# Optimization experiments

Measured on AMD Instinct MI355X. Metric: run time of the kernel, lower is better.

The kernel has to match this reference:

```python
import jax, jax.numpy as jnp
import numpy as np

B, S, D, E, K = 4, 2048, 1024, 8, 2
DF = 4 * D


def setup_inputs() -> dict:
    key = jax.random.key(0)
    ks = jax.random.split(key, 7)
    x = jax.random.normal(ks[0], (B, S, D), dtype=jnp.float32)
    Wr = jax.random.normal(ks[1], (D, E), dtype=jnp.float32) * 0.02
    br = jnp.zeros((E,), dtype=jnp.float32)
    W1 = jax.random.normal(ks[2], (E, D, DF), dtype=jnp.float32) * 0.02
    b1 = jnp.zeros((E, DF), dtype=jnp.float32)
    W2 = jax.random.normal(ks[3], (E, DF, D), dtype=jnp.float32) * 0.02
    b2 = jnp.zeros((E, D), dtype=jnp.float32)
    return {"x": x, "Wr": Wr, "br": br, "W1": W1, "b1": b1, "W2": W2, "b2": b2}


def reference(x, Wr, br, W1, b1, W2, b2):
    # Router: softmax gates then top-k
    gates = jax.nn.softmax(x @ Wr + br, axis=-1)               # [B,S,E]
    topk_vals, topk_idx = jax.lax.top_k(gates, K)              # [B,S,K]

    # Per-(token, expert) combine weight: gate value if expert selected else 0
    onehot = jax.nn.one_hot(topk_idx, E, dtype=gates.dtype)    # [B,S,K,E]
    combine = jnp.sum(onehot * topk_vals[..., None], axis=2)   # [B,S,E]

    # Expert MLPs (loop over fixed small expert count, fully vectorized per expert)
    output = jnp.zeros_like(x)
    for e in range(E):
        h = jax.nn.gelu(x @ W1[e] + b1[e], approximate=False)  # [B,S,4D]
        y = h @ W2[e] + b2[e]                                  # [B,S,D]
        output = output + combine[..., e:e + 1] * y

    # Load-balancing aux loss (dispatch mask: 1.0 where expert selected)
    dispatch = jnp.max(onehot, axis=2)                         # [B,S,E]
    mean_gates = gates.mean(axis=(0, 1))
    mean_dispatch = dispatch.mean(axis=(0, 1))
    aux_loss = jnp.sum(mean_gates * mean_dispatch) * E / (B * S)
    return output, aux_loss
```

## Files before the change

### kernel.cpp

```cpp
#include <hip/hip_runtime.h>
#include <hip/hip_bf16.h>
#include <hip/hip_fp16.h>

typedef _Float16 f16;
typedef _Float16 half8 __attribute__((ext_vector_type(8)));
typedef _Float16 half4 __attribute__((ext_vector_type(4)));
typedef float   floatx4 __attribute__((ext_vector_type(4)));

#define N_TOK   8192
#define D_DIM   1024
#define E_NUM   8
#define DF_DIM  4096
#define MAX_SLOTS 17408
#define MAX_RT    136

#define MI_COUNT  0
#define MI_CURSOR 8
#define MI_OFF    16
#define MI_TOTAL  25
#define MI_RTE    26
#define MI_SUMG   168

__device__ __forceinline__ void gld_lds16(const void* g, void* l) {
    __builtin_amdgcn_global_load_lds(
        (__attribute__((address_space(1))) const void*)g,
        (__attribute__((address_space(3))) void*)l, 16, 0, 0);
}

__device__ __forceinline__ float gelu_f(float v) {
    float u = 0.7978845608028654f * v * (1.0f + 0.044715f * v * v);
    float t = __expf(-2.0f * fabsf(u));
    float th = (1.0f - t) / (1.0f + t);
    th = (u >= 0.f) ? th : -th;
    return 0.5f * v * (1.0f + th);
}


__device__ __forceinline__ void transpose_tile(
    const float* __restrict__ src, f16* __restrict__ dst, int R, int C,
    int rb, int cb, float* tile )
{
    const int tid = threadIdx.x;
#pragma unroll
    for (int j = 0; j < 4; ++j) {
        int lin = j * 1024 + tid * 4;
        int r = lin >> 6, c = lin & 63;
        float4 v = *(const float4*)(src + (size_t)(rb + r) * C + (cb + c));
        tile[r * 65 + c + 0] = v.x; tile[r * 65 + c + 1] = v.y;
        tile[r * 65 + c + 2] = v.z; tile[r * 65 + c + 3] = v.w;
    }
    __syncthreads();
#pragma unroll
    for (int j = 0; j < 4; ++j) {
        int lin = j * 1024 + tid * 4;
        int c = lin >> 6, r = lin & 63;
        half4 o = { (f16)tile[(r + 0) * 65 + c], (f16)tile[(r + 1) * 65 + c],
                    (f16)tile[(r + 2) * 65 + c], (f16)tile[(r + 3) * 65 + c] };
        *(half4*)(dst + (size_t)(cb + c) * R + (rb + r)) = o;
    }
}

__global__ __launch_bounds__(256) void prep_kernel(
    const float* __restrict__ W1, const float* __restrict__ W2,
    f16* __restrict__ W1t, f16* __restrict__ W2t,
    const float* __restrict__ x, const float* __restrict__ Wr,
    const float* __restrict__ br,
    int* __restrict__ topk_idx, float* __restrict__ topk_w,
    int* __restrict__ meta, f16* __restrict__ xh)
{
    __shared__ float tile[64 * 65];
    __shared__ float blk_sg[E_NUM];
    __shared__ int   blk_cnt[E_NUM];

    const int bid = blockIdx.x;
    if (bid < 8192) {
        const int cx = bid & 63, ry = (bid >> 6) & 15, ez = bid >> 10;
        transpose_tile(W1 + (size_t)ez * D_DIM * DF_DIM,
                       W1t + (size_t)ez * D_DIM * DF_DIM,
                       D_DIM, DF_DIM, ry * 64, cx * 64, tile);
        return;
    }
    if (bid < 16384) {
        const int id = bid - 8192;
        const int cx = id & 15, ry = (id >> 4) & 63, ez = id >> 10;
        transpose_tile(W2 + (size_t)ez * D_DIM * DF_DIM,
                       W2t + (size_t)ez * D_DIM * DF_DIM,
                       DF_DIM, D_DIM, ry * 64, cx * 64, tile);
        return;
    }

    const int rb = bid - 16384;
    const int w = threadIdx.x >> 6, l = threadIdx.x & 63;
    if (threadIdx.x < E_NUM) { blk_sg[threadIdx.x] = 0.f; blk_cnt[threadIdx.x] = 0; }
    __syncthreads();

    for (int it = 0; it < 4; ++it) {
        const int t = rb * 16 + w * 4 + it;
        const float* xr = x + (size_t)t * D_DIM + l * 16;
        float acc[E_NUM] = {0.f,0.f,0.f,0.f,0.f,0.f,0.f,0.f};
        f16 hx[16];
#pragma unroll
        for (int i = 0; i < 16; i += 4) {
            float4 xv = *(const float4*)(xr + i);
            const float xs[4] = {xv.x, xv.y, xv.z, xv.w};
#pragma unroll
            for (int jj = 0; jj < 4; ++jj) {
                hx[i + jj] = (f16)xs[jj];
                int d = l * 16 + i + jj;
                float4 w0 = *(const float4*)(Wr + (size_t)d * 8);
                float4 w1 = *(const float4*)(Wr + (size_t)d * 8 + 4);
                acc[0] += xs[jj] * w0.x; acc[1] += xs[jj] * w0.y;
                acc[2] += xs[jj] * w0.z; acc[3] += xs[jj] * w0.w;
                acc[4] += xs[jj] * w1.x; acc[5] += xs[jj] * w1.y;
                acc[6] += xs[jj] * w1.z; acc[7] += xs[jj] * w1.w;
            }
        }
        f16* xo = xh + (size_t)t * D_DIM + l * 16;
        *(half8*)(xo)     = *(const half8*)&hx[0];
        *(half8*)(xo + 8) = *(const half8*)&hx[8];
#pragma unroll
        for (int e = 0; e < E_NUM; ++e) {
#pragma unroll
            for (int off = 32; off > 0; off >>= 1)
                acc[e] += __shfl_down(acc[e], off);
        }
        if (l == 0) {
            float lg[E_NUM], g[E_NUM];
            float mx = -1e30f;
#pragma unroll
            for (int e = 0; e < E_NUM; ++e) { lg[e] = acc[e] + br[e]; mx = fmaxf(mx, lg[e]); }
            float sum = 0.f;
#pragma unroll
            for (int e = 0; e < E_NUM; ++e) { g[e] = __expf(lg[e] - mx); sum += g[e]; }
            float inv = 1.f / sum;
#pragma unroll
            for (int e = 0; e < E_NUM; ++e) g[e] *= inv;
            int e1 = 0; float v1 = g[0];
#pragma unroll
            for (int e = 1; e < E_NUM; ++e) if (g[e] > v1) { v1 = g[e]; e1 = e; }
            int e2 = -1; float v2 = -1.f;
#pragma unroll
            for (int e = 0; e < E_NUM; ++e) if (e != e1 && g[e] > v2) { v2 = g[e]; e2 = e; }
            topk_idx[t * 2 + 0] = e1; topk_idx[t * 2 + 1] = e2;
            topk_w[t * 2 + 0] = v1;   topk_w[t * 2 + 1] = v2;
#pragma unroll
            for (int e = 0; e < E_NUM; ++e) atomicAdd(&blk_sg[e], g[e]);
            atomicAdd(&blk_cnt[e1], 1); atomicAdd(&blk_cnt[e2], 1);
        }
    }
    __syncthreads();
    if (threadIdx.x < E_NUM) {
        atomicAdd((float*)(meta + MI_SUMG) + threadIdx.x, blk_sg[threadIdx.x]);
        atomicAdd(meta + MI_COUNT + threadIdx.x, blk_cnt[threadIdx.x]);
    }
}

__global__ __launch_bounds__(256) void scan_kernel(int* __restrict__ meta, float* __restrict__ out_aux)
{
    __shared__ int offs[E_NUM + 1];
    const int tid = threadIdx.x;
    if (tid == 0) {
        int off = 0;
        for (int e = 0; e < E_NUM; ++e) {
            meta[MI_OFF + e] = off;
            offs[e] = off;
            int cnt = meta[MI_COUNT + e];
            off += ((cnt + 127) >> 7) << 7;
        }
        meta[MI_OFF + E_NUM] = off;
        offs[E_NUM] = off;
        meta[MI_TOTAL] = off >> 7;
        const float* sg = (const float*)(meta + MI_SUMG);
        float aux = 0.f;
        for (int e = 0; e < E_NUM; ++e)
            aux += (sg[e] / (float)N_TOK) * ((float)meta[MI_COUNT + e] / (float)N_TOK);
        out_aux[0] = aux * (float)E_NUM / (float)N_TOK;
    }
    __syncthreads();
    const int total = offs[E_NUM] >> 7;
    for (int rt = tid; rt < total; rt += 256) {
        int row = rt << 7, e = 0;
#pragma unroll
        for (int k = 1; k < E_NUM; ++k) if (row >= offs[k]) e = k;
        meta[MI_RTE + rt] = e;
    }
}

__global__ __launch_bounds__(256) void fill_kernel(
    const int* __restrict__ topk_idx, const float* __restrict__ topk_w,
    int* __restrict__ meta, int* __restrict__ slot_token, float* __restrict__ slot_weight,
    int* __restrict__ slot_of)
{
    int t = blockIdx.x * 256 + threadIdx.x;
#pragma unroll
    for (int k = 0; k < 2; ++k) {
        int e = topk_idx[t * 2 + k];
        int p = atomicAdd(meta + MI_CURSOR + e, 1);
        int slot = meta[MI_OFF + e] + p;
        slot_token[slot] = t;
        slot_weight[slot] = topk_w[t * 2 + k];
        slot_of[t * 2 + k] = slot;
    }
}


template<int KD, int NCOLS, int KSPLIT, bool GATHER, bool GELU, bool BIAS, bool SWZ>
__global__ __launch_bounds__(256, 4) void gemm128_kernel(
    const f16* __restrict__ A, const f16* __restrict__ Bw,
    const float* __restrict__ bias, const int* __restrict__ slot_token,
    const int* __restrict__ meta, f16* __restrict__ Out, size_t out_kp_stride)
{
    constexpr int KLOC = KD / KSPLIT;
    constexpr int NT = KLOC / 64;
    __shared__ __align__(16) f16 As[128 * 64];
    __shared__ __align__(16) f16 Bs[128 * 64];

    int nt, rt, kp;
    if (SWZ) {
        const int gx = gridDim.x, gy = gridDim.y;
        const int nwg = gx * gy * gridDim.z;
        const int flat = (blockIdx.z * gy + blockIdx.y) * gx + blockIdx.x;
        const int swz = (flat & 7) * (nwg >> 3) + (flat >> 3);
        nt = swz % gx;
        const int tmp = swz / gx;
        rt = tmp % gy;
        kp = tmp / gy;
    } else {
        nt = blockIdx.x; rt = blockIdx.y; kp = blockIdx.z;
    }

    if (rt >= meta[MI_TOTAL]) return;
    const int e  = meta[MI_RTE + rt];
    const int kbase = kp * KLOC;

    const int tid = threadIdx.x;
    const int w = tid >> 6, l = tid & 63;
    const int wr2 = w >> 1, wc2 = w & 1;
    const int fr = l & 15, fq = l >> 4;

    const int srow = tid >> 3;
    const int kcs  = (tid & 7) ^ (srow & 7);

    const f16* asrc[4]; const f16* bsrc[4];
#pragma unroll
    for (int i = 0; i < 4; ++i) {
        int r = i * 32 + srow;
        int ar;
        if (GATHER) ar = slot_token[rt * 128 + r];
        else        ar = rt * 128 + r;
        asrc[i] = A + (size_t)ar * KD + kbase + kcs * 8;
        bsrc[i] = Bw + ((size_t)e * NCOLS + (size_t)nt * 128 + r) * KD + kbase + kcs * 8;
    }

    const int rA  = wr2 * 64 + fr;
    const int rB  = wc2 * 64 + fr;
    const int sw0 = ( fq      ^ (fr & 7)) * 8;
    const int sw1 = ((4 + fq) ^ (fr & 7)) * 8;

    floatx4 acc[4][4];
#pragma unroll
    for (int m = 0; m < 4; ++m)
#pragma unroll
        for (int n = 0; n < 4; ++n) acc[m][n] = (floatx4){0.f, 0.f, 0.f, 0.f};

    half8 af[4], bf[4];

#pragma unroll 2
    for (int t = 0; t < NT; ++t) {
#pragma unroll
        for (int i = 0; i < 4; ++i) {
            gld_lds16(asrc[i] + (size_t)t * 64, &As[i * 2048 + tid * 8]);
            gld_lds16(bsrc[i] + (size_t)t * 64, &Bs[i * 2048 + tid * 8]);
        }
        asm volatile("s_waitcnt vmcnt(0)" ::: "memory");
        __builtin_amdgcn_s_barrier();
#pragma unroll
        for (int kk2 = 0; kk2 < 2; ++kk2) {
            const int sw = kk2 ? sw1 : sw0;
#pragma unroll
            for (int mj = 0; mj < 4; ++mj)
                af[mj] = *(const half8*)&As[(size_t)(rA + mj * 16) * 64 + sw];
#pragma unroll
            for (int nj = 0; nj < 4; ++nj)
                bf[nj] = *(const half8*)&Bs[(size_t)(rB + nj * 16) * 64 + sw];
#pragma unroll
            for (int mj = 0; mj < 4; ++mj)
#pragma unroll
                for (int nj = 0; nj < 4; ++nj)
                    acc[mj][nj] = __builtin_amdgcn_mfma_f32_16x16x32_f16(
                        af[mj], bf[nj], acc[mj][nj], 0, 0, 0);
        }
        __builtin_amdgcn_s_barrier();
    }

    f16* Op = Out + (size_t)kp * out_kp_stride;
    const int orow0 = rt * 128 + wr2 * 64;
    const int ocol0 = nt * 128 + wc2 * 64;
#pragma unroll
    for (int mj = 0; mj < 4; ++mj) {
#pragma unroll
        for (int nj = 0; nj < 4; ++nj) {
            const int col = ocol0 + nj * 16 + fr;
            float bs = 0.f;
            if (BIAS) bs = bias[(size_t)e * NCOLS + col];
#pragma unroll
            for (int j = 0; j < 4; ++j) {
                const int row = orow0 + mj * 16 + fq * 4 + j;
                float v = acc[mj][nj][j] + bs;
                if (GELU) v = gelu_f(v);
                Op[(size_t)row * NCOLS + col] = (f16)v;
            }
        }
    }
}

__global__ __launch_bounds__(256) void combine_kernel(
    const f16* __restrict__ P, const int* __restrict__ slot_of,
    const int* __restrict__ topk_idx, const float* __restrict__ topk_w,
    const float* __restrict__ b2, float* __restrict__ out)
{
    const int t = blockIdx.x;
    const int c = threadIdx.x;
    const size_t PS = (size_t)MAX_SLOTS * D_DIM;
    const int s0 = slot_of[t * 2], s1 = slot_of[t * 2 + 1];
    const int e0 = topk_idx[t * 2], e1 = topk_idx[t * 2 + 1];
    const float w0 = topk_w[t * 2], w1 = topk_w[t * 2 + 1];
    half4 a0 = *(const half4*)(P + (size_t)s0 * D_DIM + c * 4);
    half4 a1 = *(const half4*)(P + PS + (size_t)s0 * D_DIM + c * 4);
    half4 c0 = *(const half4*)(P + (size_t)s1 * D_DIM + c * 4);
    half4 c1 = *(const half4*)(P + PS + (size_t)s1 * D_DIM + c * 4);
    float4 bb0 = *(const float4*)(b2 + (size_t)e0 * D_DIM + c * 4);
    float4 bb1 = *(const float4*)(b2 + (size_t)e1 * D_DIM + c * 4);
    float4 o;
    o.x = w0 * ((float)a0[0] + (float)a1[0] + bb0.x) + w1 * ((float)c0[0] + (float)c1[0] + bb1.x);
    o.y = w0 * ((float)a0[1] + (float)a1[1] + bb0.y) + w1 * ((float)c0[1] + (float)c1[1] + bb1.y);
    o.z = w0 * ((float)a0[2] + (float)a1[2] + bb0.z) + w1 * ((float)c0[2] + (float)c1[2] + bb1.z);
    o.w = w0 * ((float)a0[3] + (float)a1[3] + bb0.w) + w1 * ((float)c0[3] + (float)c1[3] + bb1.w);
    *(float4*)(out + (size_t)t * D_DIM + c * 4) = o;
}

extern "C" void kernel_launch(void* const* d_in, const int* in_sizes, int n_in,
                              void* d_out, int out_size, void* d_ws, size_t ws_size,
                              hipStream_t stream) {
    const float* x  = (const float*)d_in[0];
    const float* Wr = (const float*)d_in[1];
    const float* br = (const float*)d_in[2];
    const float* W1 = (const float*)d_in[3];
    const float* b1 = (const float*)d_in[4];
    const float* W2 = (const float*)d_in[5];
    const float* b2 = (const float*)d_in[6];
    float* out = (float*)d_out;

    char* ws = (char*)d_ws;
    const size_t SZ_XH  = (size_t)N_TOK * D_DIM * 2;
    const size_t SZ_W1T = (size_t)E_NUM * DF_DIM * D_DIM * 2;
    const size_t SZ_W2T = SZ_W1T;
    const size_t SZ_H   = (size_t)MAX_SLOTS * DF_DIM * 2;

    f16* xh  = (f16*)(ws);
    f16* W1t = (f16*)(ws + SZ_XH);
    f16* W2t = (f16*)(ws + SZ_XH + SZ_W1T);
    f16* H   = (f16*)(ws + SZ_XH + SZ_W1T + SZ_W2T);
    f16* P   = (f16*)ws;
    char* p  = ws + SZ_XH + SZ_W1T + SZ_W2T + SZ_H;
    int*   topk_idx    = (int*)p;    p += (size_t)N_TOK * 2 * 4;
    float* topk_w      = (float*)p;  p += (size_t)N_TOK * 2 * 4;
    int*   slot_token  = (int*)p;    p += (size_t)MAX_SLOTS * 4;
    float* slot_weight = (float*)p;  p += (size_t)MAX_SLOTS * 4;
    int*   slot_of     = (int*)p;    p += (size_t)N_TOK * 2 * 4;
    int*   meta        = (int*)p;

    hipMemsetAsync(slot_token, 0, (size_t)MAX_SLOTS * 8 + (size_t)N_TOK * 2 * 4 + 1024, stream);

    prep_kernel<<<16896, 256, 0, stream>>>(
        W1, W2, W1t, W2t, x, Wr, br, topk_idx, topk_w, meta, xh);

    scan_kernel<<<1, 256, 0, stream>>>(meta, out + (size_t)N_TOK * D_DIM);
    fill_kernel<<<N_TOK / 256, 256, 0, stream>>>(topk_idx, topk_w, meta, slot_token, slot_weight, slot_of);

    gemm128_kernel<D_DIM, DF_DIM, 1, true, true, true, false>
        <<<dim3(DF_DIM / 128, MAX_RT, 1), 256, 0, stream>>>(
        xh, W1t, b1, slot_token, meta, H, 0);

    gemm128_kernel<DF_DIM, D_DIM, 2, false, false, false, true>
        <<<dim3(D_DIM / 128, MAX_RT, 2), 256, 0, stream>>>(
        H, W2t, nullptr, slot_token, meta, P, (size_t)MAX_SLOTS * D_DIM);

    combine_kernel<<<N_TOK, 256, 0, stream>>>(P, slot_of, topk_idx, topk_w, b2, out);

    (void)in_sizes; (void)n_in; (void)ws_size;
}
```

Before: 552.2 us.

## Move W2 transpose into first expert GEMM launch as extra blocks

The W2 fp32-to-fp16 transpose is moved out of the prep kernel and into extra blocks appended to the grid of the first expert GEMM. Those transpose blocks can then run alongside the GEMM1 tiles instead of serialising before the router and scan stages. Shared memory is unified into a raw 32KB buffer so the transpose tile (64x65 floats) fits. The risk is extra contention during GEMM1 and that the transpose blocks are scheduled after all GEMM tiles, giving little overlap.

```diff
diff --git a/kernel.cpp b/kernel.cpp
--- a/kernel.cpp
+++ b/kernel.cpp
@@ -35,7 +35,6 @@
     return 0.5f * v * (1.0f + th);
 }
 
-
 __device__ __forceinline__ void transpose_tile(
     const float* __restrict__ src, f16* __restrict__ dst, int R, int C,
     int rb, int cb, float* tile )
@@ -61,8 +60,7 @@
 }
 
 __global__ __launch_bounds__(256) void prep_kernel(
-    const float* __restrict__ W1, const float* __restrict__ W2,
-    f16* __restrict__ W1t, f16* __restrict__ W2t,
+    const float* __restrict__ W1, f16* __restrict__ W1t,
     const float* __restrict__ x, const float* __restrict__ Wr,
     const float* __restrict__ br,
     int* __restrict__ topk_idx, float* __restrict__ topk_w,
@@ -80,16 +78,8 @@
                        D_DIM, DF_DIM, ry * 64, cx * 64, tile);
         return;
     }
-    if (bid < 16384) {
-        const int id = bid - 8192;
-        const int cx = id & 15, ry = (id >> 4) & 63, ez = id >> 10;
-        transpose_tile(W2 + (size_t)ez * D_DIM * DF_DIM,
-                       W2t + (size_t)ez * D_DIM * DF_DIM,
-                       DF_DIM, D_DIM, ry * 64, cx * 64, tile);
-        return;
-    }
-
-    const int rb = bid - 16384;
+
+    const int rb = bid - 8192;
     const int w = threadIdx.x >> 6, l = threadIdx.x & 63;
     if (threadIdx.x < E_NUM) { blk_sg[threadIdx.x] = 0.f; blk_cnt[threadIdx.x] = 0; }
     __syncthreads();
@@ -204,16 +194,27 @@
 }
 
 
-template<int KD, int NCOLS, int KSPLIT, bool GATHER, bool GELU, bool BIAS, bool SWZ>
+template<int KD, int NCOLS, int KSPLIT, bool GATHER, bool GELU, bool BIAS, bool SWZ, bool FUSET>
 __global__ __launch_bounds__(256, 4) void gemm128_kernel(
     const f16* __restrict__ A, const f16* __restrict__ Bw,
     const float* __restrict__ bias, const int* __restrict__ slot_token,
-    const int* __restrict__ meta, f16* __restrict__ Out, size_t out_kp_stride)
+    const int* __restrict__ meta, f16* __restrict__ Out, size_t out_kp_stride,
+    const float* __restrict__ Tsrc, f16* __restrict__ Tdst)
 {
     constexpr int KLOC = KD / KSPLIT;
     constexpr int NT = KLOC / 64;
-    __shared__ __align__(16) f16 As[128 * 64];
-    __shared__ __align__(16) f16 Bs[128 * 64];
+    __shared__ __align__(16) char smem_raw[32768];
+    f16* As = (f16*)smem_raw;
+    f16* Bs = (f16*)(smem_raw + 16384);
+
+    if (FUSET && blockIdx.y >= MAX_RT) {
+        const int id = (blockIdx.y - MAX_RT) * gridDim.x + blockIdx.x;
+        const int cx = id & 15, ry = (id >> 4) & 63, ez = id >> 10;
+        transpose_tile(Tsrc + (size_t)ez * D_DIM * DF_DIM,
+                       Tdst + (size_t)ez * D_DIM * DF_DIM,
+                       DF_DIM, D_DIM, ry * 64, cx * 64, (float*)smem_raw);
+        return;
+    }
 
     int nt, rt, kp;
     if (SWZ) {
@@ -372,19 +373,19 @@
 
     hipMemsetAsync(slot_token, 0, (size_t)MAX_SLOTS * 8 + (size_t)N_TOK * 2 * 4 + 1024, stream);
 
-    prep_kernel<<<16896, 256, 0, stream>>>(
-        W1, W2, W1t, W2t, x, Wr, br, topk_idx, topk_w, meta, xh);
+    prep_kernel<<<8704, 256, 0, stream>>>(
+        W1, W1t, x, Wr, br, topk_idx, topk_w, meta, xh);
 
     scan_kernel<<<1, 256, 0, stream>>>(meta, out + (size_t)N_TOK * D_DIM);
     fill_kernel<<<N_TOK / 256, 256, 0, stream>>>(topk_idx, topk_w, meta, slot_token, slot_weight, slot_of);
 
-    gemm128_kernel<D_DIM, DF_DIM, 1, true, true, true, false>
-        <<<dim3(DF_DIM / 128, MAX_RT, 1), 256, 0, stream>>>(
-        xh, W1t, b1, slot_token, meta, H, 0);
-
-    gemm128_kernel<DF_DIM, D_DIM, 2, false, false, false, true>
+    gemm128_kernel<D_DIM, DF_DIM, 1, true, true, true, false, true>
+        <<<dim3(DF_DIM / 128, MAX_RT + 256, 1), 256, 0, stream>>>(
+        xh, W1t, b1, slot_token, meta, H, 0, W2, W2t);
+
+    gemm128_kernel<DF_DIM, D_DIM, 2, false, false, false, true, false>
         <<<dim3(D_DIM / 128, MAX_RT, 2), 256, 0, stream>>>(
-        H, W2t, nullptr, slot_token, meta, P, (size_t)MAX_SLOTS * D_DIM);
+        H, W2t, nullptr, slot_token, meta, P, (size_t)MAX_SLOTS * D_DIM, nullptr, nullptr);
 
     combine_kernel<<<N_TOK, 256, 0, stream>>>(P, slot_of, topk_idx, topk_w, b2, out);
 
```

Result: faster. 539.6 us (-2.3%).
